# Performance work log

Hardware: AMD Instinct MI355X
Metric: run time of the kernel (lower is better)

## Reference

```python
import jax, jax.numpy as jnp
import numpy as np
import math

B, S, D, H = 2, 2048, 2048, 16
DH = D // H  # head dim = 128
THETA = 10000.0


def _rope(x, pos):
    """Interleaved RoPE. x: [..., S, DH], pos: [S] (int)."""
    dh = x.shape[-1]
    freqs = (1.0 / THETA) ** (2.0 * jnp.arange(dh // 2, dtype=jnp.float32) / dh)  # [DH/2]
    ang = pos.astype(jnp.float32)[:, None] * freqs[None, :]  # [S, DH/2]
    cos = jnp.cos(ang).astype(x.dtype)
    sin = jnp.sin(ang).astype(x.dtype)
    xe = x[..., 0::2]
    xo = x[..., 1::2]
    oe = xe * cos - xo * sin
    oo = xe * sin + xo * cos
    return jnp.stack([oe, oo], axis=-1).reshape(x.shape)


def setup_inputs() -> dict:
    key = jax.random.key(0)
    ks = jax.random.split(key, 5)
    std = 2.0 / math.sqrt(D + D)
    x = jax.random.normal(ks[0], (B, S, D), dtype=jnp.float32)
    Wq = jax.random.normal(ks[1], (D, D), dtype=jnp.float32) * std
    Wk = jax.random.normal(ks[2], (D, D), dtype=jnp.float32) * std
    Wv = jax.random.normal(ks[3], (D, D), dtype=jnp.float32) * std
    Wo = jax.random.normal(ks[4], (D, D), dtype=jnp.float32) * std
    token_positions = jnp.arange(S, dtype=jnp.int64 if jax.config.jax_enable_x64 else jnp.int32)[None, :]
    return {"x": x, "token_positions": token_positions, "Wq": Wq, "Wk": Wk, "Wv": Wv, "Wo": Wo}


def reference(x, token_positions, Wq, Wk, Wv, Wo):
    b, s, d = x.shape
    pos = token_positions[0]  # [S]
    # QKV projections (Linear is x @ W.T, no bias)
    Q = (x @ Wq.T).reshape(b, s, H, DH).transpose(0, 2, 1, 3)  # [b,h,s,dh]
    K = (x @ Wk.T).reshape(b, s, H, DH).transpose(0, 2, 1, 3)
    V = (x @ Wv.T).reshape(b, s, H, DH).transpose(0, 2, 1, 3)
    # per-head RoPE on Q and K
    Q = _rope(Q, pos)
    K = _rope(K, pos)
    # scaled dot-product attention with causal mask
    scores = jnp.einsum('bhqd,bhkd->bhqk', Q, K) / math.sqrt(DH)
    causal = jnp.tril(jnp.ones((s, s), dtype=bool))  # [s,s]
    scores = jnp.where(causal[None, None, :, :], scores, -jnp.inf)
    prob = jax.nn.softmax(scores, axis=-1)
    O = jnp.einsum('bhqk,bhkd->bhqd', prob, V)  # [b,h,s,dh]
    O = O.transpose(0, 2, 1, 3).reshape(b, s, d)
    return O @ Wo.T
```

## Files before the change

kernel.cpp:

```cpp
#include <hip/hip_runtime.h>
#include <hip/hip_bf16.h>
#include <math.h>

#define BB 2
#define SS 2048
#define DD 2048
#define HH 16
#define DHH 128
#define MM (BB*SS)

typedef __attribute__((ext_vector_type(8))) short bf16x8;
typedef __attribute__((ext_vector_type(4))) float f32x4;

#define AS1 __attribute__((address_space(1)))
#define AS3 __attribute__((address_space(3)))
#define GLOAD_LDS16(g, l) __builtin_amdgcn_global_load_lds((const AS1 void*)(g), (AS3 void*)(l), 16, 0, 0)

#if __has_builtin(__builtin_amdgcn_exp2f)
#define EXP2F(x) __builtin_amdgcn_exp2f(x)
#else
#define EXP2F(x) exp2f(x)
#endif

__device__ __forceinline__ float b2f(short s) {
  union { unsigned int u; float f; } v;
  v.u = ((unsigned int)(unsigned short)s) << 16;
  return v.f;
}
__device__ __forceinline__ short f2b(float f) {
  union { float f; unsigned int u; } v; v.f = f;
  unsigned int u = v.u;
  u += 0x7fffu + ((u >> 16) & 1u);
  return (short)(u >> 16);
}
__device__ __forceinline__ short f2b_fast(float f) {
  union { float f; unsigned int u; } v; v.f = f;
  return (short)((v.u + 0x8000u) >> 16);
}

template<int CTRL>
__device__ __forceinline__ float dppf(float x) {
  int xi = __builtin_bit_cast(int, x);
  int r = __builtin_amdgcn_update_dpp(0, xi, CTRL, 0xf, 0xf, true);
  return __builtin_bit_cast(float, r);
}
__device__ __forceinline__ float rmax16(float x) {
  x = fmaxf(x, dppf<0xB1>(x));
  x = fmaxf(x, dppf<0x4E>(x));
  x = fmaxf(x, dppf<0x141>(x));
  x = fmaxf(x, dppf<0x140>(x));
  return x;
}
__device__ __forceinline__ float rsum16(float x) {
  x += dppf<0xB1>(x);
  x += dppf<0x4E>(x);
  x += dppf<0x141>(x);
  x += dppf<0x140>(x);
  return x;
}

__global__ void cvt_all(const float* __restrict__ x,  const float* __restrict__ wq,
                        const float* __restrict__ wk, const float* __restrict__ wv,
                        const float* __restrict__ wo,
                        short* __restrict__ xb,  short* __restrict__ wqb,
                        short* __restrict__ wkb, short* __restrict__ wvb,
                        short* __restrict__ wob) {
  int i = blockIdx.x * blockDim.x + threadIdx.x;
  const float* src; short* dst; int off;
  if (i < 2097152) { src = x; dst = xb; off = i; }
  else {
    int j = i - 2097152;
    int w = j >> 20; off = j & 1048575;
    src = (w == 0) ? wq : (w == 1) ? wk : (w == 2) ? wv : wo;
    dst = (w == 0) ? wqb : (w == 1) ? wkb : (w == 2) ? wvb : wob;
  }
  float4 v = ((const float4*)src)[i < 2097152 ? off : off];
  short4 o;
  o.x = f2b(v.x); o.y = f2b(v.y); o.z = f2b(v.z); o.w = f2b(v.w);
  ((short4*)dst)[off] = o;
}

#define LDA(cb, mt, kk) (*(const bf16x8*)((const char*)smA + (cb)*32768 + \
    (wm*128 + (mt)*16 + l16)*128 + (((kk)*64 + quad*16) ^ ((l16 & 7) << 4))))
#define LDB(cb, nt, kk) (*(const bf16x8*)((const char*)smB + (cb)*32768 + \
    (wn*64 + (nt)*16 + l16)*128 + (((kk)*64 + quad*16) ^ ((l16 & 7) << 4))))
#define STGA(b, t, h) do { \
    GLOAD_LDS16(aBase + (size_t)((h)*128) * DD + (t)*64,      smA + (b)*16384 + ((h)*128)*64 + wst); \
    GLOAD_LDS16(aBase + (size_t)((h)*128 + 64) * DD + (t)*64, smA + (b)*16384 + ((h)*128 + 64)*64 + wst); } while(0)
#define STGB(b, t, h) do { \
    GLOAD_LDS16(bBase + (size_t)((h)*128) * DD + (t)*64,      smB + (b)*16384 + ((h)*128)*64 + wst); \
    GLOAD_LDS16(bBase + (size_t)((h)*128 + 64) * DD + (t)*64, smB + (b)*16384 + ((h)*128 + 64)*64 + wst); } while(0)
#define MFMA_Q(MT0, NT0) do { \
    __builtin_amdgcn_s_setprio(1); \
    _Pragma("unroll") \
    for (int mt = 0; mt < 4; ++mt) \
      _Pragma("unroll") \
      for (int nt = 0; nt < 2; ++nt) \
        _Pragma("unroll") \
        for (int kk = 0; kk < 2; ++kk) \
          acc[(MT0) + mt][(NT0) + nt] = __builtin_amdgcn_mfma_f32_16x16x32_bf16( \
              af[mt][kk], bf[(NT0) + nt][kk], acc[(MT0) + mt][(NT0) + nt], 0, 0, 0); \
    __builtin_amdgcn_s_setprio(0); } while(0)

__global__ __launch_bounds__(512, 2)
void gemm_qkv(const short* __restrict__ A,
              const short* __restrict__ Wq, const short* __restrict__ Wk,
              const short* __restrict__ Wv, const int* __restrict__ pos,
              short* __restrict__ Qo, short* __restrict__ Ko, short* __restrict__ Vo) {
  __shared__ __align__(16) short sm[65536];
  const int tid = threadIdx.x;
  const int lane = tid & 63;
  const int wave = tid >> 6;
  const int quad = lane >> 4, l16 = lane & 15;
  const int wm = wave >> 2, wn = wave & 3;
  const int wsel = blockIdx.x >> 3;
  const short* Bw = (wsel == 0) ? Wq : (wsel == 1) ? Wk : Wv;
  short* Cout = (wsel == 0) ? Qo : (wsel == 1) ? Ko : Vo;
  const int bn = (blockIdx.x & 7) * 256;
  const int bm = blockIdx.y * 256;

  short* smA = sm;
  short* smB = sm + 32768;
  const int wst = wave * 512;

  const int srow = tid >> 3;
  const int scol = ((tid & 7) ^ (srow & 7)) * 8;
  const short* aBase = A  + (size_t)(bm + srow) * DD + scol;
  const short* bBase = Bw + (size_t)(bn + srow) * DD + scol;

  f32x4 acc[8][4] = {};
  bf16x8 af[4][2], bf[4][2];

  STGA(0, 0, 0); STGA(0, 0, 1);
  STGB(0, 0, 0); STGB(0, 0, 1);
  STGB(1, 1, 0); STGB(1, 1, 1);
  asm volatile("s_waitcnt vmcnt(4)" ::: "memory");
  __builtin_amdgcn_s_barrier();

  for (int t = 0; t < 32; ++t) {
    const int cb = t & 1, nb = cb ^ 1;
    #pragma unroll
    for (int mt = 0; mt < 4; ++mt) { af[mt][0] = LDA(cb, mt, 0); af[mt][1] = LDA(cb, mt, 1); }
    #pragma unroll
    for (int nt = 0; nt < 2; ++nt) { bf[nt][0] = LDB(cb, nt, 0); bf[nt][1] = LDB(cb, nt, 1); }
    if (t + 1 < 32) STGA(nb, t + 1, 0);
    __builtin_amdgcn_s_barrier();
    asm volatile("s_waitcnt lgkmcnt(0)" ::: "memory");
    __builtin_amdgcn_sched_barrier(0);
    MFMA_Q(0, 0);
    __builtin_amdgcn_s_barrier();
    #pragma unroll
    for (int nt = 2; nt < 4; ++nt) { bf[nt][0] = LDB(cb, nt, 0); bf[nt][1] = LDB(cb, nt, 1); }
    if (t + 1 < 32) STGA(nb, t + 1, 1);
    __builtin_amdgcn_s_barrier();
    asm volatile("s_waitcnt lgkmcnt(0)" ::: "memory");
    __builtin_amdgcn_sched_barrier(0);
    MFMA_Q(0, 2);
    __builtin_amdgcn_s_barrier();
    #pragma unroll
    for (int mt = 0; mt < 4; ++mt) { af[mt][0] = LDA(cb, mt + 4, 0); af[mt][1] = LDA(cb, mt + 4, 1); }
    if (t + 2 < 32) STGB(cb, t + 2, 0);
    __builtin_amdgcn_s_barrier();
    asm volatile("s_waitcnt lgkmcnt(0)" ::: "memory");
    __builtin_amdgcn_sched_barrier(0);
    MFMA_Q(4, 2);
    __builtin_amdgcn_s_barrier();
    if (t + 2 < 32) {
      STGB(cb, t + 2, 1);
      asm volatile("s_waitcnt vmcnt(4)" ::: "memory");
    } else {
      asm volatile("s_waitcnt vmcnt(0)" ::: "memory");
    }
    __builtin_amdgcn_s_barrier();
    MFMA_Q(4, 0);
    __builtin_amdgcn_s_barrier();
  }

  if (wsel < 2) {
    const float post = (wsel == 0) ? 0.1275174306f : 1.0f;
    float fr[4];
    #pragma unroll
    for (int nt = 0; nt < 4; ++nt) {
      int pi = (wn & 1) * 32 + nt * 8 + (l16 >> 1);
      fr[nt] = __expf(-0.14391156831f * (float)pi);
    }
    const float sgn = (l16 & 1) ? 1.0f : -1.0f;
    #pragma unroll
    for (int mt = 0; mt < 8; ++mt) {
      #pragma unroll
      for (int r = 0; r < 4; ++r) {
        int m = bm + wm*128 + mt*16 + quad*4 + r;
        float fp = (float)pos[m & 2047];
        #pragma unroll
        for (int nt = 0; nt < 4; ++nt) {
          float v = acc[mt][nt][r];
          float p = dppf<0xB1>(v);
          float ang = fp * fr[nt];
          float sn = __sinf(ang), cs = __cosf(ang);
          acc[mt][nt][r] = (v * cs + sgn * p * sn) * post;
        }
      }
    }
  }

  #pragma unroll
  for (int mt = 0; mt < 8; ++mt)
    #pragma unroll
    for (int nt = 0; nt < 4; ++nt)
      #pragma unroll
      for (int r = 0; r < 4; ++r) {
        int m = bm + wm*128 + mt*16 + quad*4 + r;
        int n = bn + wn*64 + nt*16 + l16;
        int b = m >> 11, s = m & 2047;
        int h = n >> 7,  d = n & 127;
        Cout[(((size_t)(b*HH + h)*SS + s)*DHH) + d] = f2b(acc[mt][nt][r]);
      }
}

__global__ __launch_bounds__(256)
void gemm_o(const short* __restrict__ A, const short* __restrict__ Bw,
            float* __restrict__ Cout) {
  __shared__ __align__(16) short As[128*64];
  __shared__ __align__(16) short Bs[128*64];
  const int tid = threadIdx.x;
  const int lane = tid & 63;
  const int wave = tid >> 6;
  const int wm = wave >> 1, wn = wave & 1;
  const int quad = lane >> 4, l16 = lane & 15;
  const int bm = blockIdx.y * 128, bn = blockIdx.x * 128;
  const int K = DD;

  const int srow = tid >> 3;
  const int scol = (tid & 7) * 8;
  const short* aBase = A + (size_t)(bm + srow) * K + scol;
  const short* bBase = Bw + (size_t)(bn + srow) * K + scol;
  f32x4 acc[4][4] = {};

  for (int k0 = 0; k0 < K; k0 += 64) {
    #pragma unroll
    for (int j = 0; j < 4; ++j) {
      GLOAD_LDS16(aBase + (size_t)j * 32 * K + k0, As + j * 2048 + wave * 512);
      GLOAD_LDS16(bBase + (size_t)j * 32 * K + k0, Bs + j * 2048 + wave * 512);
    }
    __syncthreads();
    #pragma unroll
    for (int kk = 0; kk < 64; kk += 32) {
      bf16x8 af[4], bf[4];
      #pragma unroll
      for (int t = 0; t < 4; ++t)
        af[t] = *(const bf16x8*)&As[(wm*64 + t*16 + l16) * 64 + kk + quad*8];
      #pragma unroll
      for (int t = 0; t < 4; ++t)
        bf[t] = *(const bf16x8*)&Bs[(wn*64 + t*16 + l16) * 64 + kk + quad*8];
      #pragma unroll
      for (int mt = 0; mt < 4; ++mt)
        #pragma unroll
        for (int nt = 0; nt < 4; ++nt)
          acc[mt][nt] = __builtin_amdgcn_mfma_f32_16x16x32_bf16(af[mt], bf[nt], acc[mt][nt], 0, 0, 0);
    }
    __syncthreads();
  }

  #pragma unroll
  for (int mt = 0; mt < 4; ++mt)
    #pragma unroll
    for (int nt = 0; nt < 4; ++nt)
      #pragma unroll
      for (int r = 0; r < 4; ++r) {
        int m = bm + wm*64 + mt*16 + quad*4 + r;
        int n = bn + wn*64 + nt*16 + l16;
        Cout[(size_t)m * DD + n] = acc[mt][nt][r];
      }
}

__global__ __launch_bounds__(256, 3)
void attn(const short* __restrict__ Q, const short* __restrict__ K,
          const short* __restrict__ V, short* __restrict__ O) {
  __shared__ __align__(16) short Ks[64*128];
  __shared__ __align__(16) short Vt[128*64];
  __shared__ __align__(16) short Pb[4*16*64];
  const int tid = threadIdx.x;
  const int lane = tid & 63, wave = tid >> 6;
  const int quad = lane >> 4, l16 = lane & 15;
  const int L = blockIdx.x;
  const int bh = L & 31;
  const int s = L >> 5;
  const int qt = (s < 8) ? 31 - s : (s < 16) ? s - 8 : (s < 24) ? 39 - s : s - 16;
  const int b = bh >> 4, h = bh & 15;
  const short* Kg = K + (size_t)bh * SS * DHH;
  const short* Vg = V + (size_t)bh * SS * DHH;
  const int qbase = qt * 64 + wave * 16;

  bf16x8 aq[4];
  {
    const short* qp = Q + ((size_t)bh * SS + qbase + l16) * DHH + quad*8;
    #pragma unroll
    for (int ks = 0; ks < 4; ++ks) aq[ks] = *(const bf16x8*)(qp + ks*32);
  }

  f32x4 o[8] = {};
  float mrow[4], lrow[4];
  #pragma unroll
  for (int r = 0; r < 4; ++r) { mrow[r] = -1e30f; lrow[r] = 0.f; }

  const int skey0 = wave*16 + (lane >> 4);
  const int scolb = (lane & 15) << 4;
  const int vkp = (tid & 31) * 2;
  const int vds = (tid >> 5) * 16;

  const int nkt = qt + 1;
  int4 vreg[4];
  {
    const short* vp = Vg + (size_t)vkp * DHH + vds;
    vreg[0] = *(const int4*)vp;         vreg[1] = *(const int4*)(vp + 8);
    vreg[2] = *(const int4*)(vp + DHH); vreg[3] = *(const int4*)(vp + DHH + 8);
  }

  for (int kt = 0; kt < nkt; ++kt) {
    {
      const short* Kt = Kg + (size_t)kt * 64 * DHH;
      #pragma unroll
      for (int j = 0; j < 4; ++j) {
        int key = skey0 + j*4;
        GLOAD_LDS16(Kt + (size_t)key * DHH + ((scolb ^ ((key & 7) << 4)) >> 1),
                    Ks + wave*2048 + j*512);
      }
    }
    asm volatile("" ::: "memory");
    {
      const short* s0 = (const short*)&vreg[0];
      const short* s1 = (const short*)&vreg[2];
      #pragma unroll
      for (int e = 0; e < 16; ++e) {
        int dim = vds + e;
        int val = (int)(unsigned short)s0[e] | ((int)(unsigned short)s1[e] << 16);
        *(int*)((char*)Vt + dim*128 + ((vkp*2) ^ ((dim & 7) << 4))) = val;
      }
    }
    if (kt + 1 < nkt) {
      const short* vp = Vg + (size_t)((kt+1)*64 + vkp) * DHH + vds;
      vreg[0] = *(const int4*)vp;         vreg[1] = *(const int4*)(vp + 8);
      vreg[2] = *(const int4*)(vp + DHH); vreg[3] = *(const int4*)(vp + DHH + 8);
      asm volatile("s_waitcnt vmcnt(4) lgkmcnt(0)" ::: "memory");
    } else {
      asm volatile("s_waitcnt vmcnt(0) lgkmcnt(0)" ::: "memory");
    }
    __builtin_amdgcn_s_barrier();
    __builtin_amdgcn_sched_barrier(0);

    float sv[4][4];
    __builtin_amdgcn_s_setprio(1);
    #pragma unroll
    for (int nt = 0; nt < 4; ++nt) {
      f32x4 a = {0.f, 0.f, 0.f, 0.f};
      #pragma unroll
      for (int ks = 0; ks < 4; ++ks) {
        int key = nt*16 + l16;
        bf16x8 bk = *(const bf16x8*)((const char*)Ks + key*256 +
                       ((ks*64 + quad*16) ^ ((key & 7) << 4)));
        a = __builtin_amdgcn_mfma_f32_16x16x32_bf16(aq[ks], bk, a, 0, 0, 0);
      }
      #pragma unroll
      for (int r = 0; r < 4; ++r) sv[nt][r] = a[r];
    }
    __builtin_amdgcn_s_setprio(0);

    if (kt == qt) {
      #pragma unroll
      for (int nt = 0; nt < 4; ++nt)
        #pragma unroll
        for (int r = 0; r < 4; ++r)
          if (nt*16 + l16 > wave*16 + quad*4 + r) sv[nt][r] = -1e30f;
    }

    #pragma unroll
    for (int r = 0; r < 4; ++r) {
      float mx = fmaxf(fmaxf(sv[0][r], sv[1][r]), fmaxf(sv[2][r], sv[3][r]));
      mx = rmax16(mx);
      float mnew = fmaxf(mrow[r], mx);
      float alpha = EXP2F(mrow[r] - mnew);
      float ls = 0.f;
      #pragma unroll
      for (int nt = 0; nt < 4; ++nt) {
        float pv = EXP2F(sv[nt][r] - mnew);
        sv[nt][r] = pv; ls += pv;
      }
      ls = rsum16(ls);
      lrow[r] = lrow[r] * alpha + ls;
      mrow[r] = mnew;
      #pragma unroll
      for (int nt = 0; nt < 8; ++nt) o[nt][r] *= alpha;
    }

    #pragma unroll
    for (int nt = 0; nt < 4; ++nt)
      #pragma unroll
      for (int r = 0; r < 4; ++r) {
        int qr = quad*4 + r;
        *(short*)((char*)Pb + wave*2048 + qr*128 +
                  (((nt*16 + l16)*2) ^ ((qr & 7) << 4))) = f2b_fast(sv[nt][r]);
      }

    bf16x8 ap[2];
    #pragma unroll
    for (int k2 = 0; k2 < 2; ++k2)
      ap[k2] = *(const bf16x8*)((const char*)Pb + wave*2048 + l16*128 +
                  ((k2*64 + quad*16) ^ ((l16 & 7) << 4)));

    __builtin_amdgcn_s_setprio(1);
    #pragma unroll
    for (int k2 = 0; k2 < 2; ++k2)
      #pragma unroll
      for (int nt = 0; nt < 8; ++nt) {
        int d = nt*16 + l16;
        bf16x8 bv = *(const bf16x8*)((const char*)Vt + d*128 +
                       ((k2*64 + quad*16) ^ ((d & 7) << 4)));
        o[nt] = __builtin_amdgcn_mfma_f32_16x16x32_bf16(ap[k2], bv, o[nt], 0, 0, 0);
      }
    __builtin_amdgcn_s_setprio(0);

    asm volatile("s_waitcnt lgkmcnt(0)" ::: "memory");
    __builtin_amdgcn_s_barrier();
    __builtin_amdgcn_sched_barrier(0);
  }

  #pragma unroll
  for (int nt = 0; nt < 8; ++nt)
    #pragma unroll
    for (int r = 0; r < 4; ++r) {
      int q = qbase + quad*4 + r;
      float v = o[nt][r] / lrow[r];
      O[((size_t)(b*SS + q)) * DD + h*DHH + nt*16 + l16] = f2b(v);
    }
}

extern "C" void kernel_launch(void* const* d_in, const int* in_sizes, int n_in,
                              void* d_out, int out_size, void* d_ws, size_t ws_size,
                              hipStream_t stream) {
  const float* x  = (const float*)d_in[0];
  const int* pos  = (const int*)d_in[1];
  const float* Wq = (const float*)d_in[2];
  const float* Wk = (const float*)d_in[3];
  const float* Wv = (const float*)d_in[4];
  const float* Wo = (const float*)d_in[5];

  char* ws = (char*)d_ws;
  short* xb  = (short*)(ws);
  short* wqb = (short*)(ws + 16777216);
  short* wkb = (short*)(ws + 25165824);
  short* wvb = (short*)(ws + 33554432);
  short* wob = (short*)(ws + 41943040);
  short* Qb  = (short*)(ws + 50331648);
  short* Kb  = (short*)(ws + 67108864);
  short* Vb  = (short*)(ws + 83886080);
  short* Ob  = (short*)(ws + 100663296);

  cvt_all<<<24576, 256, 0, stream>>>(x, Wq, Wk, Wv, Wo, xb, wqb, wkb, wvb, wob);

  dim3 gq(24, MM/256);
  gemm_qkv<<<gq, 512, 0, stream>>>(xb, wqb, wkb, wvb, pos, Qb, Kb, Vb);

  attn<<<1024, 256, 0, stream>>>(Qb, Kb, Vb, Ob);

  dim3 go(DD/128, MM/128);
  gemm_o<<<go, 256, 0, stream>>>(Ob, wob, (float*)d_out);
}
```

Measured before the change: 398.8 us.

## Retile QKV and O GEMMs to 256x128 with shared triple-buffered B pipeline

Both the QKV projection and the output projection GEMMs now use a shared 256x128 block tile with 8 waves (64x64 per wave). The K-loop double-buffers A and triple-buffers B through direct global-to-LDS loads with XOR swizzling. Block indices are remapped so that blocks launched close together on an XCD share tiles, which should improve L2 reuse. This replaces the simple synchronous 128x128 gemm_o, but the QKV kernel now uses smaller per-wave tiles, so arithmetic intensity per wave drops and the block count grows.

```diff
diff --git a/kernel.cpp b/kernel.cpp
--- a/kernel.cpp
+++ b/kernel.cpp
@@ -80,17 +80,19 @@
   ((short4*)dst)[off] = o;
 }
 
-#define LDA(cb, mt, kk) (*(const bf16x8*)((const char*)smA + (cb)*32768 + \
-    (wm*128 + (mt)*16 + l16)*128 + (((kk)*64 + quad*16) ^ ((l16 & 7) << 4))))
-#define LDB(cb, nt, kk) (*(const bf16x8*)((const char*)smB + (cb)*32768 + \
-    (wn*64 + (nt)*16 + l16)*128 + (((kk)*64 + quad*16) ^ ((l16 & 7) << 4))))
-#define STGA(b, t, h) do { \
-    GLOAD_LDS16(aBase + (size_t)((h)*128) * DD + (t)*64,      smA + (b)*16384 + ((h)*128)*64 + wst); \
-    GLOAD_LDS16(aBase + (size_t)((h)*128 + 64) * DD + (t)*64, smA + (b)*16384 + ((h)*128 + 64)*64 + wst); } while(0)
-#define STGB(b, t, h) do { \
-    GLOAD_LDS16(bBase + (size_t)((h)*128) * DD + (t)*64,      smB + (b)*16384 + ((h)*128)*64 + wst); \
-    GLOAD_LDS16(bBase + (size_t)((h)*128 + 64) * DD + (t)*64, smB + (b)*16384 + ((h)*128 + 64)*64 + wst); } while(0)
-#define MFMA_Q(MT0, NT0) do { \
+#define LDA2(cb, mt, kk) (*(const bf16x8*)((const char*)smA + (cb)*32768 + \
+    (wm*64 + (mt)*16 + l16)*128 + ((((kk)*64) + quad*16) ^ ((l16 & 7) << 4))))
+#define LDB3(b, nt, kk) (*(const bf16x8*)((const char*)smB + (b)*16384 + \
+    (wn*64 + (nt)*16 + l16)*128 + ((((kk)*64) + quad*16) ^ ((l16 & 7) << 4))))
+#define STGA4(b, t) do { \
+    _Pragma("unroll") \
+    for (int h = 0; h < 4; ++h) \
+      GLOAD_LDS16(aBase + (size_t)(h*64) * DD + (t)*64, smA + (b)*16384 + h*4096 + wst); } while(0)
+#define STGB2M(b, t) do { \
+    _Pragma("unroll") \
+    for (int h = 0; h < 2; ++h) \
+      GLOAD_LDS16(bBase + (size_t)(h*64) * DD + (t)*64, smB + (b)*8192 + h*4096 + wst); } while(0)
+#define MFMA_P(NT0) do { \
     __builtin_amdgcn_s_setprio(1); \
     _Pragma("unroll") \
     for (int mt = 0; mt < 4; ++mt) \
@@ -98,26 +100,63 @@
       for (int nt = 0; nt < 2; ++nt) \
         _Pragma("unroll") \
         for (int kk = 0; kk < 2; ++kk) \
-          acc[(MT0) + mt][(NT0) + nt] = __builtin_amdgcn_mfma_f32_16x16x32_bf16( \
-              af[mt][kk], bf[(NT0) + nt][kk], acc[(MT0) + mt][(NT0) + nt], 0, 0, 0); \
+          acc[mt][(NT0) + nt] = __builtin_amdgcn_mfma_f32_16x16x32_bf16( \
+              af[mt][kk], bf[(NT0) + nt][kk], acc[mt][(NT0) + nt], 0, 0, 0); \
     __builtin_amdgcn_s_setprio(0); } while(0)
+
+#define GEMM_KLOOP \
+  STGA4(0, 0); STGB2M(0, 0); STGB2M(1, 1); \
+  asm volatile("s_waitcnt vmcnt(2)" ::: "memory"); \
+  __builtin_amdgcn_s_barrier(); \
+  int b3 = 0, b3n2 = 2; \
+  for (int t = 0; t < 32; ++t) { \
+    const int cb = t & 1, nb = cb ^ 1; \
+    _Pragma("unroll") \
+    for (int mt = 0; mt < 4; ++mt) { af[mt][0] = LDA2(cb, mt, 0); af[mt][1] = LDA2(cb, mt, 1); } \
+    _Pragma("unroll") \
+    for (int nt = 0; nt < 2; ++nt) { bf[nt][0] = LDB3(b3, nt, 0); bf[nt][1] = LDB3(b3, nt, 1); } \
+    if (t + 1 < 32) STGA4(nb, t + 1); \
+    __builtin_amdgcn_s_barrier(); \
+    asm volatile("s_waitcnt lgkmcnt(0)" ::: "memory"); \
+    __builtin_amdgcn_sched_barrier(0); \
+    MFMA_P(0); \
+    __builtin_amdgcn_s_barrier(); \
+    _Pragma("unroll") \
+    for (int nt = 2; nt < 4; ++nt) { bf[nt][0] = LDB3(b3, nt, 0); bf[nt][1] = LDB3(b3, nt, 1); } \
+    if (t + 2 < 32) { \
+      STGB2M(b3n2, t + 2); \
+      asm volatile("s_waitcnt vmcnt(2)" ::: "memory"); \
+    } else { \
+      asm volatile("s_waitcnt vmcnt(0)" ::: "memory"); \
+    } \
+    __builtin_amdgcn_s_barrier(); \
+    asm volatile("s_waitcnt lgkmcnt(0)" ::: "memory"); \
+    __builtin_amdgcn_sched_barrier(0); \
+    MFMA_P(2); \
+    __builtin_amdgcn_s_barrier(); \
+    b3 = (b3 == 2) ? 0 : b3 + 1; \
+    b3n2 = (b3n2 == 2) ? 0 : b3n2 + 1; \
+  }
 
 __global__ __launch_bounds__(512, 2)
 void gemm_qkv(const short* __restrict__ A,
               const short* __restrict__ Wq, const short* __restrict__ Wk,
               const short* __restrict__ Wv, const int* __restrict__ pos,
               short* __restrict__ Qo, short* __restrict__ Ko, short* __restrict__ Vo) {
-  __shared__ __align__(16) short sm[65536];
+  __shared__ __align__(16) short sm[57344];
   const int tid = threadIdx.x;
   const int lane = tid & 63;
   const int wave = tid >> 6;
   const int quad = lane >> 4, l16 = lane & 15;
-  const int wm = wave >> 2, wn = wave & 3;
-  const int wsel = blockIdx.x >> 3;
+  const int wm = wave >> 1, wn = wave & 1;
+
+  const int wid = (blockIdx.x & 7) * 96 + (blockIdx.x >> 3);
+  const int wsel = wid >> 8;
+  const int idr = wid & 255;
+  const int bm = (idr >> 4) * 256;
+  const int bn = (idr & 15) * 128;
   const short* Bw = (wsel == 0) ? Wq : (wsel == 1) ? Wk : Wv;
   short* Cout = (wsel == 0) ? Qo : (wsel == 1) ? Ko : Vo;
-  const int bn = (blockIdx.x & 7) * 256;
-  const int bm = blockIdx.y * 256;
 
   short* smA = sm;
   short* smB = sm + 32768;
@@ -128,68 +167,25 @@
   const short* aBase = A  + (size_t)(bm + srow) * DD + scol;
   const short* bBase = Bw + (size_t)(bn + srow) * DD + scol;
 
-  f32x4 acc[8][4] = {};
+  f32x4 acc[4][4] = {};
   bf16x8 af[4][2], bf[4][2];
 
-  STGA(0, 0, 0); STGA(0, 0, 1);
-  STGB(0, 0, 0); STGB(0, 0, 1);
-  STGB(1, 1, 0); STGB(1, 1, 1);
-  asm volatile("s_waitcnt vmcnt(4)" ::: "memory");
-  __builtin_amdgcn_s_barrier();
-
-  for (int t = 0; t < 32; ++t) {
-    const int cb = t & 1, nb = cb ^ 1;
-    #pragma unroll
-    for (int mt = 0; mt < 4; ++mt) { af[mt][0] = LDA(cb, mt, 0); af[mt][1] = LDA(cb, mt, 1); }
-    #pragma unroll
-    for (int nt = 0; nt < 2; ++nt) { bf[nt][0] = LDB(cb, nt, 0); bf[nt][1] = LDB(cb, nt, 1); }
-    if (t + 1 < 32) STGA(nb, t + 1, 0);
-    __builtin_amdgcn_s_barrier();
-    asm volatile("s_waitcnt lgkmcnt(0)" ::: "memory");
-    __builtin_amdgcn_sched_barrier(0);
-    MFMA_Q(0, 0);
-    __builtin_amdgcn_s_barrier();
-    #pragma unroll
-    for (int nt = 2; nt < 4; ++nt) { bf[nt][0] = LDB(cb, nt, 0); bf[nt][1] = LDB(cb, nt, 1); }
-    if (t + 1 < 32) STGA(nb, t + 1, 1);
-    __builtin_amdgcn_s_barrier();
-    asm volatile("s_waitcnt lgkmcnt(0)" ::: "memory");
-    __builtin_amdgcn_sched_barrier(0);
-    MFMA_Q(0, 2);
-    __builtin_amdgcn_s_barrier();
-    #pragma unroll
-    for (int mt = 0; mt < 4; ++mt) { af[mt][0] = LDA(cb, mt + 4, 0); af[mt][1] = LDA(cb, mt + 4, 1); }
-    if (t + 2 < 32) STGB(cb, t + 2, 0);
-    __builtin_amdgcn_s_barrier();
-    asm volatile("s_waitcnt lgkmcnt(0)" ::: "memory");
-    __builtin_amdgcn_sched_barrier(0);
-    MFMA_Q(4, 2);
-    __builtin_amdgcn_s_barrier();
-    if (t + 2 < 32) {
-      STGB(cb, t + 2, 1);
-      asm volatile("s_waitcnt vmcnt(4)" ::: "memory");
-    } else {
-      asm volatile("s_waitcnt vmcnt(0)" ::: "memory");
-    }
-    __builtin_amdgcn_s_barrier();
-    MFMA_Q(4, 0);
-    __builtin_amdgcn_s_barrier();
-  }
+  GEMM_KLOOP
 
   if (wsel < 2) {
     const float post = (wsel == 0) ? 0.1275174306f : 1.0f;
     float fr[4];
     #pragma unroll
     for (int nt = 0; nt < 4; ++nt) {
-      int pi = (wn & 1) * 32 + nt * 8 + (l16 >> 1);
+      int pi = wn * 32 + nt * 8 + (l16 >> 1);
       fr[nt] = __expf(-0.14391156831f * (float)pi);
     }
     const float sgn = (l16 & 1) ? 1.0f : -1.0f;
     #pragma unroll
-    for (int mt = 0; mt < 8; ++mt) {
+    for (int mt = 0; mt < 4; ++mt) {
       #pragma unroll
       for (int r = 0; r < 4; ++r) {
-        int m = bm + wm*128 + mt*16 + quad*4 + r;
+        int m = bm + wm*64 + mt*16 + quad*4 + r;
         float fp = (float)pos[m & 2047];
         #pragma unroll
         for (int nt = 0; nt < 4; ++nt) {
@@ -204,12 +200,12 @@
   }
 
   #pragma unroll
-  for (int mt = 0; mt < 8; ++mt)
+  for (int mt = 0; mt < 4; ++mt)
     #pragma unroll
     for (int nt = 0; nt < 4; ++nt)
       #pragma unroll
       for (int r = 0; r < 4; ++r) {
-        int m = bm + wm*128 + mt*16 + quad*4 + r;
+        int m = bm + wm*64 + mt*16 + quad*4 + r;
         int n = bn + wn*64 + nt*16 + l16;
         int b = m >> 11, s = m & 2047;
         int h = n >> 7,  d = n & 127;
@@ -217,49 +213,33 @@
       }
 }
 
-__global__ __launch_bounds__(256)
+__global__ __launch_bounds__(512, 2)
 void gemm_o(const short* __restrict__ A, const short* __restrict__ Bw,
             float* __restrict__ Cout) {
-  __shared__ __align__(16) short As[128*64];
-  __shared__ __align__(16) short Bs[128*64];
+  __shared__ __align__(16) short sm[57344];
   const int tid = threadIdx.x;
   const int lane = tid & 63;
   const int wave = tid >> 6;
+  const int quad = lane >> 4, l16 = lane & 15;
   const int wm = wave >> 1, wn = wave & 1;
-  const int quad = lane >> 4, l16 = lane & 15;
-  const int bm = blockIdx.y * 128, bn = blockIdx.x * 128;
-  const int K = DD;
+
+  const int wid = (blockIdx.x & 7) * 32 + (blockIdx.x >> 3);
+  const int bm = (wid >> 4) * 256;
+  const int bn = (wid & 15) * 128;
+
+  short* smA = sm;
+  short* smB = sm + 32768;
+  const int wst = wave * 512;
 
   const int srow = tid >> 3;
-  const int scol = (tid & 7) * 8;
-  const short* aBase = A + (size_t)(bm + srow) * K + scol;
-  const short* bBase = Bw + (size_t)(bn + srow) * K + scol;
+  const int scol = ((tid & 7) ^ (srow & 7)) * 8;
+  const short* aBase = A  + (size_t)(bm + srow) * DD + scol;
+  const short* bBase = Bw + (size_t)(bn + srow) * DD + scol;
+
   f32x4 acc[4][4] = {};
-
-  for (int k0 = 0; k0 < K; k0 += 64) {
-    #pragma unroll
-    for (int j = 0; j < 4; ++j) {
-      GLOAD_LDS16(aBase + (size_t)j * 32 * K + k0, As + j * 2048 + wave * 512);
-      GLOAD_LDS16(bBase + (size_t)j * 32 * K + k0, Bs + j * 2048 + wave * 512);
-    }
-    __syncthreads();
-    #pragma unroll
-    for (int kk = 0; kk < 64; kk += 32) {
-      bf16x8 af[4], bf[4];
-      #pragma unroll
-      for (int t = 0; t < 4; ++t)
-        af[t] = *(const bf16x8*)&As[(wm*64 + t*16 + l16) * 64 + kk + quad*8];
-      #pragma unroll
-      for (int t = 0; t < 4; ++t)
-        bf[t] = *(const bf16x8*)&Bs[(wn*64 + t*16 + l16) * 64 + kk + quad*8];
-      #pragma unroll
-      for (int mt = 0; mt < 4; ++mt)
-        #pragma unroll
-        for (int nt = 0; nt < 4; ++nt)
-          acc[mt][nt] = __builtin_amdgcn_mfma_f32_16x16x32_bf16(af[mt], bf[nt], acc[mt][nt], 0, 0, 0);
-    }
-    __syncthreads();
-  }
+  bf16x8 af[4][2], bf[4][2];
+
+  GEMM_KLOOP
 
   #pragma unroll
   for (int mt = 0; mt < 4; ++mt)
@@ -457,11 +437,9 @@
 
   cvt_all<<<24576, 256, 0, stream>>>(x, Wq, Wk, Wv, Wo, xb, wqb, wkb, wvb, wob);
 
-  dim3 gq(24, MM/256);
-  gemm_qkv<<<gq, 512, 0, stream>>>(xb, wqb, wkb, wvb, pos, Qb, Kb, Vb);
+  gemm_qkv<<<768, 512, 0, stream>>>(xb, wqb, wkb, wvb, pos, Qb, Kb, Vb);
 
   attn<<<1024, 256, 0, stream>>>(Qb, Kb, Vb, Ob);
 
-  dim3 go(DD/128, MM/128);
-  gemm_o<<<go, 256, 0, stream>>>(Ob, wob, (float*)d_out);
-}
+  gemm_o<<<256, 512, 0, stream>>>(Ob, wob, (float*)d_out);
+}
```

Measured after the change: 380.5 us. -4.6%, faster.
